# Kernel optimization log

Measured on AMD Instinct MI355X. Metric: run time of the kernel, lower is better.

Reference implementation:

```python
import jax, jax.numpy as jnp
import numpy as np

B, S, E = 2, 2048, 1024
H, D = 16, 64  # num_heads, head_size; H*D == E

def setup_inputs() -> dict:
    key = jax.random.key(0)
    k1, k2, k3 = jax.random.split(key, 3)
    x = jax.random.normal(k1, (B, S, E), dtype=jnp.float32)
    w_qkv = jax.random.normal(k2, (E, 3 * H * D), dtype=jnp.float32) / np.sqrt(E)
    b_qkv = jnp.zeros((3 * H * D,), dtype=jnp.float32)
    w_out = jax.random.normal(k3, (H * D, E), dtype=jnp.float32) / np.sqrt(H * D)
    b_out = jnp.zeros((E,), dtype=jnp.float32)
    return {"x": x, "w_qkv": w_qkv, "b_qkv": b_qkv, "w_out": w_out, "b_out": b_out}

def reference(x, w_qkv, b_qkv, w_out, b_out):
    b, s, e = x.shape
    qkv = x @ w_qkv + b_qkv                       # [b, s, 3*H*D]
    qkv = qkv.reshape(b, s, 3, H, D).transpose(2, 0, 3, 1, 4)  # [3, b, H, s, D]
    q, k, v = qkv[0], qkv[1], qkv[2]
    scores = jnp.einsum('bhqd,bhkd->bhqk', q, k) / jnp.sqrt(jnp.float32(D))
    mask = jnp.tril(jnp.ones((s, s), dtype=scores.dtype))
    scores = scores * mask - 1e10 * (1 - mask)
    attn = jax.nn.softmax(scores, axis=-1)
    out = jnp.einsum('bhqk,bhkd->bhqd', attn, v)  # [b, H, s, D]
    out = out.transpose(0, 2, 1, 3).reshape(b, s, H * D)
    return out @ w_out + b_out
```

## Files before the change

### kernel.cpp

```cpp
#include <hip/hip_runtime.h>

typedef unsigned short u16;
typedef __attribute__((ext_vector_type(8))) short bf16x8;
typedef __attribute__((ext_vector_type(4))) float f32x4;

#define S_LEN 2048
#define MTOT  4096
#define LOG2E_DIV8 0.1803368784f

__device__ inline u16 f2bf(float f) {
  union { float f; unsigned u; } x; x.f = f;
  unsigned r = x.u + 0x7fffu + ((x.u >> 16) & 1u);
  return (u16)(r >> 16);
}

__device__ __forceinline__ unsigned cvtpk_bf16(float lo, float hi) {
  unsigned r;
  asm("v_cvt_pk_bf16_f32 %0, %1, %2" : "=v"(r) : "v"(lo), "v"(hi));
  return r;
}
__device__ __forceinline__ float fexp2(float x) {
  float r;
  asm("v_exp_f32 %0, %1" : "=v"(r) : "v"(x));
  return r;
}
__device__ __forceinline__ float frcp(float x) {
  float r;
  asm("v_rcp_f32 %0, %1" : "=v"(r) : "v"(x));
  return r;
}

typedef __attribute__((address_space(1))) const unsigned int gu32;
typedef __attribute__((address_space(3))) unsigned int lu32;
__device__ __forceinline__ void gload_lds16(const void* g, void* l) {
  __builtin_amdgcn_global_load_lds((gu32*)g, (lu32*)l, 16, 0, 0);
}

#define MFMA16(a, b, c) __builtin_amdgcn_mfma_f32_16x16x32_bf16((a), (b), (c), 0, 0, 0)

__global__ __launch_bounds__(256) void cast_bf16(const float* __restrict__ src,
                                                 u16* __restrict__ dst, int n) {
  int i = (blockIdx.x * 256 + threadIdx.x) * 4;
  if (i >= n) return;
  float4 v = *(const float4*)(src + i);
  ushort4 o;
  o.x = f2bf(v.x); o.y = f2bf(v.y); o.z = f2bf(v.z); o.w = f2bf(v.w);
  *(ushort4*)(dst + i) = o;
}

__global__ __launch_bounds__(256) void transcast(const float* __restrict__ src,
                                                 u16* __restrict__ dst, int K, int N) {
  __shared__ float tile[64][65];
  int n0 = blockIdx.x * 64, k0 = blockIdx.y * 64;
  int t = threadIdx.x;
  for (int i = 0; i < 16; ++i) {
    int idx = t + 256 * i;
    int r = idx >> 6, c = idx & 63;
    tile[r][c] = src[(size_t)(k0 + r) * N + n0 + c];
  }
  __syncthreads();
  for (int i = 0; i < 16; ++i) {
    int idx = t + 256 * i;
    int r = idx >> 6, c = idx & 63;
    dst[(size_t)(n0 + r) * K + k0 + c] = f2bf(tile[c][r]);
  }
}

template<int OUT_BF16>
__global__ __launch_bounds__(256) void gemm_bt(const u16* __restrict__ A,
                                               const u16* __restrict__ Bt,
                                               const float* __restrict__ bias,
                                               void* __restrict__ Cv,
                                               int N, int K,
                                               int qcols, float qscale) {
  __shared__ __align__(16) u16 As[128 * 32];
  __shared__ __align__(16) u16 Bs[128 * 32];
  int t = threadIdx.x;
  int w = t >> 6, l = t & 63;
  int wr = w >> 1, wc = w & 1;
  int lr = l & 15, lg = l >> 4;

  int nwg = gridDim.x * gridDim.y;
  int bid = blockIdx.y * gridDim.x + blockIdx.x;
  int orig = (bid & 7) * (nwg >> 3) + (bid >> 3);
  int bx = orig % gridDim.x, by = orig / gridDim.x;
  int m0 = by * 128, n0 = bx * 128;

  f32x4 acc[4][4];
#pragma unroll
  for (int i = 0; i < 4; ++i)
#pragma unroll
    for (int j = 0; j < 4; ++j)
      acc[i][j] = f32x4{0.f, 0.f, 0.f, 0.f};

  int r0 = w * 32 + (l >> 2);
  int r1 = r0 + 16;
  int c0 = (l & 3) ^ ((r0 >> 1) & 3);
  int c1 = (l & 3) ^ ((r1 >> 1) & 3);
  const u16* gA0 = A + (size_t)(m0 + r0) * K + c0 * 8;
  const u16* gA1 = A + (size_t)(m0 + r1) * K + c1 * 8;
  const u16* gB0 = Bt + (size_t)(n0 + r0) * K + c0 * 8;
  const u16* gB1 = Bt + (size_t)(n0 + r1) * K + c1 * 8;
  u16* lA0 = As + (w * 32) * 32;
  u16* lA1 = As + (w * 32 + 16) * 32;
  u16* lB0 = Bs + (w * 32) * 32;
  u16* lB1 = Bs + (w * 32 + 16) * 32;

  for (int k0 = 0; k0 < K; k0 += 32) {
    gload_lds16(gA0 + k0, lA0);
    gload_lds16(gA1 + k0, lA1);
    gload_lds16(gB0 + k0, lB0);
    gload_lds16(gB1 + k0, lB1);
    __syncthreads();
    bf16x8 af[4], bfr[4];
#pragma unroll
    for (int mi = 0; mi < 4; ++mi) {
      int row = wr * 64 + mi * 16 + lr;
      af[mi] = *(const bf16x8*)(As + row * 32 + ((lg ^ ((row >> 1) & 3)) << 3));
    }
#pragma unroll
    for (int ni = 0; ni < 4; ++ni) {
      int row = wc * 64 + ni * 16 + lr;
      bfr[ni] = *(const bf16x8*)(Bs + row * 32 + ((lg ^ ((row >> 1) & 3)) << 3));
    }
    __builtin_amdgcn_s_setprio(1);
#pragma unroll
    for (int mi = 0; mi < 4; ++mi)
#pragma unroll
      for (int ni = 0; ni < 4; ++ni)
        acc[mi][ni] = MFMA16(af[mi], bfr[ni], acc[mi][ni]);
    __builtin_amdgcn_s_setprio(0);
    __syncthreads();
  }

#pragma unroll
  for (int mi = 0; mi < 4; ++mi)
#pragma unroll
    for (int ni = 0; ni < 4; ++ni)
#pragma unroll
      for (int rg = 0; rg < 4; ++rg) {
        int row = m0 + wr * 64 + mi * 16 + lg * 4 + rg;
        int col = n0 + wc * 64 + ni * 16 + lr;
        float v = acc[mi][ni][rg] + bias[col];
        if (col < qcols) v *= qscale;
        if (OUT_BF16) ((u16*)Cv)[(size_t)row * N + col] = f2bf(v);
        else          ((float*)Cv)[(size_t)row * N + col] = v;
      }
}

__global__ __launch_bounds__(256) void vtrans(const u16* __restrict__ qkv,
                                              u16* __restrict__ Vt) {
  __shared__ __align__(16) u16 tile[64][72];
  int s0 = blockIdx.x * 64;
  int bh = blockIdx.y;
  int b = bh >> 4, h = bh & 15;
  int t = threadIdx.x;
  for (int c = 0; c < 2; ++c) {
    int idx = t + 256 * c;
    int r = idx >> 3, off = (idx & 7) * 8;
    *(uint4*)(&tile[r][off]) =
        *(const uint4*)(qkv + (size_t)(b * S_LEN + s0 + r) * 3072 + 2048 + h * 64 + off);
  }
  __syncthreads();
  int d = t >> 2, sb = (t & 3) * 16;
  __align__(16) u16 tmp[16];
  for (int j = 0; j < 16; ++j) tmp[j] = tile[sb + j][d];
  u16* dst = Vt + (size_t)(bh * 64 + d) * S_LEN + s0 + sb;
  *(uint4*)(dst) = *(uint4*)(tmp);
  *(uint4*)(dst + 8) = *(uint4*)(tmp + 8);
}


__device__ __forceinline__ void softmax_update(f32x4* s, float& l_run) {
  float ps = 0.f;
#pragma unroll
  for (int ct = 0; ct < 4; ++ct)
#pragma unroll
    for (int rg = 0; rg < 4; ++rg) {
      float p = fexp2(s[ct][rg]);
      s[ct][rg] = p;
      ps += p;
    }
  ps += __shfl_xor(ps, 16);
  ps += __shfl_xor(ps, 32);
  l_run += ps;
}

__device__ __forceinline__ void p_store(f32x4* s, u16* Psw, int lr, int lg) {
#pragma unroll
  for (int ct = 0; ct < 4; ++ct) {
    uint2 pk;
    pk.x = cvtpk_bf16(s[ct][0], s[ct][1]);
    pk.y = cvtpk_bf16(s[ct][2], s[ct][3]);
    *(uint2*)(Psw + lr * 72 + ct * 16 + lg * 4) = pk;
  }
}

__device__ __forceinline__ void attn_tile(const u16* Ks, const u16* Vs, u16* Psw,
                                          bf16x8 q0, bf16x8 q1, f32x4* o,
                                          float& l_run, bool diag,
                                          int w, int l, int lr, int lg) {
  f32x4 s[4];
  __builtin_amdgcn_s_setprio(1);
#pragma unroll
  for (int ct = 0; ct < 4; ++ct) {
    int row = ct * 16 + lr;
    bf16x8 kf0 = *(const bf16x8*)(Ks + ((row * 64 + lg * 8) ^ ((row & 7) << 3)));
    bf16x8 kf1 = *(const bf16x8*)(Ks + ((row * 64 + 32 + lg * 8) ^ ((row & 7) << 3)));
    f32x4 z = f32x4{0.f, 0.f, 0.f, 0.f};
    z = MFMA16(kf0, q0, z);
    z = MFMA16(kf1, q1, z);
    s[ct] = z;
  }
  __builtin_amdgcn_s_setprio(0);
  if (diag) {
    int qrel = w * 16 + lr;
#pragma unroll
    for (int ct = 0; ct < 4; ++ct)
#pragma unroll
      for (int rg = 0; rg < 4; ++rg)
        if ((ct * 16 + lg * 4 + rg) > qrel) s[ct][rg] = -1e30f;
  }
  softmax_update(s, l_run);
  p_store(s, Psw, lr, lg);
  bf16x8 pf0 = *(const bf16x8*)(Psw + lr * 72 + lg * 8);
  bf16x8 pf1 = *(const bf16x8*)(Psw + lr * 72 + 32 + lg * 8);
  __builtin_amdgcn_s_setprio(1);
#pragma unroll
  for (int dt = 0; dt < 4; ++dt) {
    int row = dt * 16 + lr;
    bf16x8 vf0 = *(const bf16x8*)(Vs + ((row * 64 + lg * 8) ^ ((row & 7) << 3)));
    bf16x8 vf1 = *(const bf16x8*)(Vs + ((row * 64 + 32 + lg * 8) ^ ((row & 7) << 3)));
    o[dt] = MFMA16(pf0, vf0, o[dt]);
    o[dt] = MFMA16(pf1, vf1, o[dt]);
  }
  __builtin_amdgcn_s_setprio(0);
}

__global__ __launch_bounds__(256) void attn_kernel(const u16* __restrict__ qkv,
                                                   const u16* __restrict__ Vt,
                                                   u16* __restrict__ attnb) {
  __shared__ __align__(16) u16 Ks[2][64 * 64];
  __shared__ __align__(16) u16 Vs[2][64 * 64];
  __shared__ __align__(16) u16 PsA[4][16 * 72];
  __shared__ __align__(16) u16 PsB[4][16 * 72];
  int bid = blockIdx.y * 16 + blockIdx.x;
  int orig = (bid & 7) * 64 + (bid >> 3);
  int qtA = orig & 15, bh = orig >> 4;
  int qtB = 31 - qtA;
  int b = bh >> 4, h = bh & 15;
  int t = threadIdx.x, w = t >> 6, l = t & 63;
  int lr = l & 15, lg = l >> 4;

  const u16* qbase = qkv + (size_t)b * S_LEN * 3072 + h * 64;
  int qrA = qtA * 64 + w * 16 + lr;
  int qrB = qtB * 64 + w * 16 + lr;
  bf16x8 qA0 = *(const bf16x8*)(qbase + (size_t)qrA * 3072 + lg * 8);
  bf16x8 qA1 = *(const bf16x8*)(qbase + (size_t)qrA * 3072 + 32 + lg * 8);
  bf16x8 qB0 = *(const bf16x8*)(qbase + (size_t)qrB * 3072 + lg * 8);
  bf16x8 qB1 = *(const bf16x8*)(qbase + (size_t)qrB * 3072 + 32 + lg * 8);

  f32x4 oA[4], oB[4];
#pragma unroll
  for (int i = 0; i < 4; ++i) { oA[i] = f32x4{0.f,0.f,0.f,0.f}; oB[i] = f32x4{0.f,0.f,0.f,0.f}; }
  float lA = 0.f, lB = 0.f;

  int r0s = t >> 3, r1s = r0s + 32;
  int soff = (t & 7) * 8;
  int e0 = (r0s * 64 + soff) ^ ((r0s & 7) << 3);
  int e1 = (r1s * 64 + soff) ^ ((r1s & 7) << 3);
  const u16* Kg = qkv + (size_t)b * S_LEN * 3072 + 1024 + h * 64 + soff;
  const u16* Vg = Vt + (size_t)bh * 64 * S_LEN + soff;

  uint4 k0r, k1r, v0r, v1r;
#define ISSUE(KT) {                                                     \
    int kk0 = (KT) * 64;                                                \
    k0r = *(const uint4*)(Kg + (size_t)(kk0 + r0s) * 3072);             \
    k1r = *(const uint4*)(Kg + (size_t)(kk0 + r1s) * 3072);             \
    v0r = *(const uint4*)(Vg + (size_t)r0s * S_LEN + kk0);              \
    v1r = *(const uint4*)(Vg + (size_t)r1s * S_LEN + kk0);              }

  int nkt = qtB + 1;
  ISSUE(0);
  *(uint4*)(Ks[0] + e0) = k0r;
  *(uint4*)(Ks[0] + e1) = k1r;
  *(uint4*)(Vs[0] + e0) = v0r;
  *(uint4*)(Vs[0] + e1) = v1r;
  ISSUE(1);
  __syncthreads();

  int cur = 0;
  for (int kt = 0; kt < nkt; ++kt) {
    if (kt + 1 < nkt) {
      u16* Kd = Ks[cur ^ 1];
      u16* Vd = Vs[cur ^ 1];
      *(uint4*)(Kd + e0) = k0r;
      *(uint4*)(Kd + e1) = k1r;
      *(uint4*)(Vd + e0) = v0r;
      *(uint4*)(Vd + e1) = v1r;
    }
    if (kt + 2 < nkt) ISSUE(kt + 2);
    const u16* Kc = Ks[cur];
    const u16* Vc = Vs[cur];
    if (kt <= qtA)
      attn_tile(Kc, Vc, &PsA[w][0], qA0, qA1, oA, lA, kt == qtA, w, l, lr, lg);
    attn_tile(Kc, Vc, &PsB[w][0], qB0, qB1, oB, lB, kt == qtB, w, l, lr, lg);
    __syncthreads();
    cur ^= 1;
  }
#undef ISSUE

  float lqA[4], lqB[4];
#pragma unroll
  for (int rg = 0; rg < 4; ++rg) {
    lqA[rg] = frcp(__shfl(lA, (l & 48) | (lg * 4 + rg)));
    lqB[rg] = frcp(__shfl(lB, (l & 48) | (lg * 4 + rg)));
  }
#pragma unroll
  for (int dt = 0; dt < 4; ++dt)
#pragma unroll
    for (int rg = 0; rg < 4; ++rg) {
      int d = dt * 16 + lr;
      int qA_ = qtA * 64 + w * 16 + lg * 4 + rg;
      int qB_ = qtB * 64 + w * 16 + lg * 4 + rg;
      attnb[(size_t)(b * S_LEN + qA_) * 1024 + h * 64 + d] = f2bf(oA[dt][rg] * lqA[rg]);
      attnb[(size_t)(b * S_LEN + qB_) * 1024 + h * 64 + d] = f2bf(oB[dt][rg] * lqB[rg]);
    }
}

extern "C" void kernel_launch(void* const* d_in, const int* in_sizes, int n_in,
                              void* d_out, int out_size, void* d_ws, size_t ws_size,
                              hipStream_t stream) {
  const float* x     = (const float*)d_in[0];
  const float* w_qkv = (const float*)d_in[1];
  const float* b_qkv = (const float*)d_in[2];
  const float* w_out = (const float*)d_in[3];
  const float* b_out = (const float*)d_in[4];
  float* out = (float*)d_out;

  char* ws = (char*)d_ws;
  u16* x_bf   = (u16*)(ws);
  u16* wqkvT  = (u16*)(ws + ( 8ull << 20));
  u16* woutT  = (u16*)(ws + (14ull << 20));
  u16* qkv    = (u16*)(ws + (16ull << 20));
  u16* Vt     = (u16*)(ws + (40ull << 20));
  u16* attnb  = (u16*)(ws + (48ull << 20));

  cast_bf16<<<MTOT * 1024 / 1024, 256, 0, stream>>>(x, x_bf, MTOT * 1024);
  transcast<<<dim3(48, 16), 256, 0, stream>>>(w_qkv, wqkvT, 1024, 3072);
  transcast<<<dim3(16, 16), 256, 0, stream>>>(w_out, woutT, 1024, 1024);
  gemm_bt<1><<<dim3(24, 32), 256, 0, stream>>>(x_bf, wqkvT, b_qkv, (void*)qkv,
                                               3072, 1024, 1024, LOG2E_DIV8);
  vtrans<<<dim3(32, 32), 256, 0, stream>>>(qkv, Vt);
  attn_kernel<<<dim3(16, 32), 256, 0, stream>>>(qkv, Vt, attnb);
  gemm_bt<0><<<dim3(8, 32), 256, 0, stream>>>(attnb, woutT, b_out, (void*)out,
                                              1024, 1024, 0, 1.0f);
}
```

Baseline: 118.0 us.

## Split attention KV range across two blocks and combine partial outputs

Each query-tile pair is now split across two blocks, each covering half of the key tiles. The halves write unnormalized bf16 partial outputs and row sums, and a new combine kernel adds them and normalizes. The change also replaces the LDS round trip used to reshape P with register permlane swaps, uses permlane swaps for the row-sum reduction, and sets a min-blocks launch bound of 4. This doubles the grid to improve occupancy and load balance, at the cost of an extra kernel, extra memory traffic, and rounding the partial sums to bf16 before they are combined.

```diff
diff --git a/kernel.cpp b/kernel.cpp
--- a/kernel.cpp
+++ b/kernel.cpp
@@ -13,6 +13,10 @@
   unsigned r = x.u + 0x7fffu + ((x.u >> 16) & 1u);
   return (u16)(r >> 16);
 }
+__device__ inline float bf2f(u16 u) {
+  union { unsigned u; float f; } x; x.u = ((unsigned)u) << 16;
+  return x.f;
+}
 
 __device__ __forceinline__ unsigned cvtpk_bf16(float lo, float hi) {
   unsigned r;
@@ -28,6 +32,18 @@
   float r;
   asm("v_rcp_f32 %0, %1" : "=v"(r) : "v"(x));
   return r;
+}
+
+#define SWAP32(a, b) asm("v_permlane32_swap_b32 %0, %1" : "+v"(a), "+v"(b))
+#define SWAP16(a, b) asm("v_permlane16_swap_b32 %0, %1" : "+v"(a), "+v"(b))
+
+__device__ __forceinline__ float sum_lg(float x) {
+  float a = x, b = x;
+  SWAP32(a, b);
+  float s = a + b;
+  float c = s, d = s;
+  SWAP16(c, d);
+  return c + d;
 }
 
 typedef __attribute__((address_space(1))) const unsigned int gu32;
@@ -170,33 +186,7 @@
   *(uint4*)(dst + 8) = *(uint4*)(tmp + 8);
 }
 
-
-__device__ __forceinline__ void softmax_update(f32x4* s, float& l_run) {
-  float ps = 0.f;
-#pragma unroll
-  for (int ct = 0; ct < 4; ++ct)
-#pragma unroll
-    for (int rg = 0; rg < 4; ++rg) {
-      float p = fexp2(s[ct][rg]);
-      s[ct][rg] = p;
-      ps += p;
-    }
-  ps += __shfl_xor(ps, 16);
-  ps += __shfl_xor(ps, 32);
-  l_run += ps;
-}
-
-__device__ __forceinline__ void p_store(f32x4* s, u16* Psw, int lr, int lg) {
-#pragma unroll
-  for (int ct = 0; ct < 4; ++ct) {
-    uint2 pk;
-    pk.x = cvtpk_bf16(s[ct][0], s[ct][1]);
-    pk.y = cvtpk_bf16(s[ct][2], s[ct][3]);
-    *(uint2*)(Psw + lr * 72 + ct * 16 + lg * 4) = pk;
-  }
-}
-
-__device__ __forceinline__ void attn_tile(const u16* Ks, const u16* Vs, u16* Psw,
+__device__ __forceinline__ void attn_tile(const u16* Ks, const u16* Vs,
                                           bf16x8 q0, bf16x8 q1, f32x4* o,
                                           float& l_run, bool diag,
                                           int w, int l, int lr, int lg) {
@@ -221,33 +211,61 @@
       for (int rg = 0; rg < 4; ++rg)
         if ((ct * 16 + lg * 4 + rg) > qrel) s[ct][rg] = -1e30f;
   }
-  softmax_update(s, l_run);
-  p_store(s, Psw, lr, lg);
-  bf16x8 pf0 = *(const bf16x8*)(Psw + lr * 72 + lg * 8);
-  bf16x8 pf1 = *(const bf16x8*)(Psw + lr * 72 + 32 + lg * 8);
+  float ps = 0.f;
+#pragma unroll
+  for (int ct = 0; ct < 4; ++ct)
+#pragma unroll
+    for (int rg = 0; rg < 4; ++rg) {
+      float p = fexp2(s[ct][rg]);
+      s[ct][rg] = p;
+      ps += p;
+    }
+  l_run += sum_lg(ps);
+
+  unsigned W00 = cvtpk_bf16(s[0][0], s[0][1]);
+  unsigned W01 = cvtpk_bf16(s[0][2], s[0][3]);
+  unsigned W10 = cvtpk_bf16(s[1][0], s[1][1]);
+  unsigned W11 = cvtpk_bf16(s[1][2], s[1][3]);
+  unsigned W20 = cvtpk_bf16(s[2][0], s[2][1]);
+  unsigned W21 = cvtpk_bf16(s[2][2], s[2][3]);
+  unsigned W30 = cvtpk_bf16(s[3][0], s[3][1]);
+  unsigned W31 = cvtpk_bf16(s[3][2], s[3][3]);
+  SWAP32(W00, W10); SWAP16(W00, W10);
+  SWAP32(W01, W11); SWAP16(W01, W11);
+  SWAP32(W20, W30); SWAP16(W20, W30);
+  SWAP32(W21, W31); SWAP16(W21, W31);
+  union { unsigned u[4]; bf16x8 v; } P0, P1;
+  P0.u[0] = W00; P0.u[1] = W01; P0.u[2] = W10; P0.u[3] = W11;
+  P1.u[0] = W20; P1.u[1] = W21; P1.u[2] = W30; P1.u[3] = W31;
+
   __builtin_amdgcn_s_setprio(1);
 #pragma unroll
   for (int dt = 0; dt < 4; ++dt) {
     int row = dt * 16 + lr;
     bf16x8 vf0 = *(const bf16x8*)(Vs + ((row * 64 + lg * 8) ^ ((row & 7) << 3)));
     bf16x8 vf1 = *(const bf16x8*)(Vs + ((row * 64 + 32 + lg * 8) ^ ((row & 7) << 3)));
-    o[dt] = MFMA16(pf0, vf0, o[dt]);
-    o[dt] = MFMA16(pf1, vf1, o[dt]);
+    o[dt] = MFMA16(P0.v, vf0, o[dt]);
+    o[dt] = MFMA16(P1.v, vf1, o[dt]);
   }
   __builtin_amdgcn_s_setprio(0);
 }
 
-__global__ __launch_bounds__(256) void attn_kernel(const u16* __restrict__ qkv,
-                                                   const u16* __restrict__ Vt,
-                                                   u16* __restrict__ attnb) {
+__global__ __launch_bounds__(256, 4) void attn_kernel(const u16* __restrict__ qkv,
+                                                      const u16* __restrict__ Vt,
+                                                      u16* __restrict__ po0,
+                                                      u16* __restrict__ po1,
+                                                      float* __restrict__ pl) {
   __shared__ __align__(16) u16 Ks[2][64 * 64];
   __shared__ __align__(16) u16 Vs[2][64 * 64];
-  __shared__ __align__(16) u16 PsA[4][16 * 72];
-  __shared__ __align__(16) u16 PsB[4][16 * 72];
-  int bid = blockIdx.y * 16 + blockIdx.x;
-  int orig = (bid & 7) * 64 + (bid >> 3);
-  int qtA = orig & 15, bh = orig >> 4;
+  int bid = blockIdx.y * 32 + blockIdx.x;
+  int orig = (bid & 7) * 128 + (bid >> 3);
+  int half = orig & 1;
+  int qtA = (orig >> 1) & 15;
+  int bh = orig >> 5;
   int qtB = 31 - qtA;
+  int m = (qtA >= 8) ? 8 : (15 - qtA);
+  int kts = half ? m : 0;
+  int kte = half ? (qtB + 1) : m;
   int b = bh >> 4, h = bh & 15;
   int t = threadIdx.x, w = t >> 6, l = t & 63;
   int lr = l & 15, lg = l >> 4;
@@ -280,18 +298,17 @@
     v0r = *(const uint4*)(Vg + (size_t)r0s * S_LEN + kk0);              \
     v1r = *(const uint4*)(Vg + (size_t)r1s * S_LEN + kk0);              }
 
-  int nkt = qtB + 1;
-  ISSUE(0);
+  ISSUE(kts);
   *(uint4*)(Ks[0] + e0) = k0r;
   *(uint4*)(Ks[0] + e1) = k1r;
   *(uint4*)(Vs[0] + e0) = v0r;
   *(uint4*)(Vs[0] + e1) = v1r;
-  ISSUE(1);
+  if (kts + 1 < kte) ISSUE(kts + 1);
   __syncthreads();
 
   int cur = 0;
-  for (int kt = 0; kt < nkt; ++kt) {
-    if (kt + 1 < nkt) {
+  for (int kt = kts; kt < kte; ++kt) {
+    if (kt + 1 < kte) {
       u16* Kd = Ks[cur ^ 1];
       u16* Vd = Vs[cur ^ 1];
       *(uint4*)(Kd + e0) = k0r;
@@ -299,23 +316,19 @@
       *(uint4*)(Vd + e0) = v0r;
       *(uint4*)(Vd + e1) = v1r;
     }
-    if (kt + 2 < nkt) ISSUE(kt + 2);
+    if (kt + 2 < kte) ISSUE(kt + 2);
     const u16* Kc = Ks[cur];
     const u16* Vc = Vs[cur];
     if (kt <= qtA)
-      attn_tile(Kc, Vc, &PsA[w][0], qA0, qA1, oA, lA, kt == qtA, w, l, lr, lg);
-    attn_tile(Kc, Vc, &PsB[w][0], qB0, qB1, oB, lB, kt == qtB, w, l, lr, lg);
+      attn_tile(Kc, Vc, qA0, qA1, oA, lA, kt == qtA, w, l, lr, lg);
+    attn_tile(Kc, Vc, qB0, qB1, oB, lB, kt == qtB, w, l, lr, lg);
     __syncthreads();
     cur ^= 1;
   }
 #undef ISSUE
 
-  float lqA[4], lqB[4];
-#pragma unroll
-  for (int rg = 0; rg < 4; ++rg) {
-    lqA[rg] = frcp(__shfl(lA, (l & 48) | (lg * 4 + rg)));
-    lqB[rg] = frcp(__shfl(lB, (l & 48) | (lg * 4 + rg)));
-  }
+  u16* po = half ? po1 : po0;
+  float* plh = pl + half * 65536;
 #pragma unroll
   for (int dt = 0; dt < 4; ++dt)
 #pragma unroll
@@ -323,9 +336,32 @@
       int d = dt * 16 + lr;
       int qA_ = qtA * 64 + w * 16 + lg * 4 + rg;
       int qB_ = qtB * 64 + w * 16 + lg * 4 + rg;
-      attnb[(size_t)(b * S_LEN + qA_) * 1024 + h * 64 + d] = f2bf(oA[dt][rg] * lqA[rg]);
-      attnb[(size_t)(b * S_LEN + qB_) * 1024 + h * 64 + d] = f2bf(oB[dt][rg] * lqB[rg]);
-    }
+      po[(size_t)(b * S_LEN + qA_) * 1024 + h * 64 + d] = f2bf(oA[dt][rg]);
+      po[(size_t)(b * S_LEN + qB_) * 1024 + h * 64 + d] = f2bf(oB[dt][rg]);
+    }
+  if (lg == 0) {
+    plh[bh * 2048 + qtA * 64 + w * 16 + lr] = lA;
+    plh[bh * 2048 + qtB * 64 + w * 16 + lr] = lB;
+  }
+}
+
+__global__ __launch_bounds__(256) void attn_combine(const u16* po0,
+                                                    const u16* __restrict__ po1,
+                                                    const float* __restrict__ pl,
+                                                    u16* out) {
+  int i = (blockIdx.x * 256 + threadIdx.x) * 8;
+  int row = i >> 10;
+  int h = (i & 1023) >> 6;
+  int bh = (row >> 11) * 16 + h;
+  int q = row & 2047;
+  float r = frcp(pl[bh * 2048 + q] + pl[65536 + bh * 2048 + q]);
+  bf16x8 a = *(const bf16x8*)(po0 + i);
+  bf16x8 c = *(const bf16x8*)(po1 + i);
+  union { u16 u[8]; bf16x8 v; } o;
+#pragma unroll
+  for (int j = 0; j < 8; ++j)
+    o.u[j] = f2bf((bf2f((u16)a[j]) + bf2f((u16)c[j])) * r);
+  *(bf16x8*)(out + i) = o.v;
 }
 
 extern "C" void kernel_launch(void* const* d_in, const int* in_sizes, int n_in,
@@ -340,10 +376,13 @@
 
   char* ws = (char*)d_ws;
   u16* x_bf   = (u16*)(ws);
+  u16* po1    = (u16*)(ws);
   u16* wqkvT  = (u16*)(ws + ( 8ull << 20));
+  float* pl   = (float*)(ws + ( 8ull << 20));
   u16* woutT  = (u16*)(ws + (14ull << 20));
   u16* qkv    = (u16*)(ws + (16ull << 20));
   u16* Vt     = (u16*)(ws + (40ull << 20));
+  u16* po0    = (u16*)(ws + (48ull << 20));
   u16* attnb  = (u16*)(ws + (48ull << 20));
 
   cast_bf16<<<MTOT * 1024 / 1024, 256, 0, stream>>>(x, x_bf, MTOT * 1024);
@@ -352,7 +391,8 @@
   gemm_bt<1><<<dim3(24, 32), 256, 0, stream>>>(x_bf, wqkvT, b_qkv, (void*)qkv,
                                                3072, 1024, 1024, LOG2E_DIV8);
   vtrans<<<dim3(32, 32), 256, 0, stream>>>(qkv, Vt);
-  attn_kernel<<<dim3(16, 32), 256, 0, stream>>>(qkv, Vt, attnb);
+  attn_kernel<<<dim3(32, 32), 256, 0, stream>>>(qkv, Vt, po0, po1, pl);
+  attn_combine<<<MTOT * 1024 / (256 * 8), 256, 0, stream>>>(po0, po1, pl, attnb);
   gemm_bt<0><<<dim3(8, 32), 256, 0, stream>>>(attnb, woutT, b_out, (void*)out,
                                               1024, 1024, 0, 1.0f);
 }
```

Measured after the change: 118.5 us. Within noise of the previous version (+0.4%).
